# Performance work log

Hardware: AMD Instinct MI355X
Metric: run time of the kernel (lower is better)

Reference implementation:

```python
import jax, jax.numpy as jnp
import numpy as np

NUM_ITEMS = 200000
B = 512
S = 64
D = 64
H = 1
NBLOCKS = 2
EPS = 1e-3  # keras LayerNormalization default epsilon
NEG = -2.0 ** 32 + 1.0  # padding value used by SASRec multihead_attention


def setup_inputs() -> dict:
    key = jax.random.key(0)
    ks = jax.random.split(key, 12)

    def nrm(k, shape, s=0.02):
        return jax.random.normal(k, shape, dtype=jnp.float32) * s

    return {
        "input_ids": jax.random.randint(ks[0], (B, S), 0, NUM_ITEMS + 1),  # id == NUM_ITEMS is padding
        "item_emb": nrm(ks[1], (NUM_ITEMS + 1, D)),
        "pos_emb": nrm(ks[2], (S, D)),
        "ln1_g": jnp.ones((NBLOCKS, D), jnp.float32),
        "ln1_b": jnp.zeros((NBLOCKS, D), jnp.float32),
        "Wq": nrm(ks[3], (NBLOCKS, D, D)),
        "bq": jnp.zeros((NBLOCKS, D), jnp.float32),
        "Wk": nrm(ks[4], (NBLOCKS, D, D)),
        "bk": jnp.zeros((NBLOCKS, D), jnp.float32),
        "Wv": nrm(ks[5], (NBLOCKS, D, D)),
        "bv": jnp.zeros((NBLOCKS, D), jnp.float32),
        "ln2_g": jnp.ones((NBLOCKS, D), jnp.float32),
        "ln2_b": jnp.zeros((NBLOCKS, D), jnp.float32),
        "W1": nrm(ks[6], (NBLOCKS, D, D)),
        "b1": jnp.zeros((NBLOCKS, D), jnp.float32),
        "W2": nrm(ks[7], (NBLOCKS, D, D)),
        "b2": jnp.zeros((NBLOCKS, D), jnp.float32),
        "lnf_g": jnp.ones((D,), jnp.float32),
        "lnf_b": jnp.zeros((D,), jnp.float32),
        "out_item_emb": nrm(ks[8], (NUM_ITEMS, D)),
    }


def _layernorm(x, g, b):
    mu = jnp.mean(x, -1, keepdims=True)
    var = jnp.var(x, -1, keepdims=True)
    return (x - mu) * jax.lax.rsqrt(var + EPS) * g + b


def _mha(queries, keys, Wq, bq, Wk, bk, Wv, bv):
    # SASRec-style multihead attention (inference: dropout disabled).
    # Head split/merge via reshape == tf.split/concat along batch in original.
    Bq, Sq, Dm = queries.shape
    dh = Dm // H

    def split(x):  # [B,S,D] -> [B,H,S,dh]
        return x.reshape(Bq, Sq, H, dh).transpose(0, 2, 1, 3)

    Q = split(queries @ Wq + bq)
    K = split(keys @ Wk + bk)
    V = split(keys @ Wv + bv)
    scores = jnp.einsum('bhqd,bhkd->bhqk', Q, K) / jnp.sqrt(jnp.float32(dh))
    # key masking: padded key positions (all-zero embeddings) get -inf
    key_mask = jnp.sign(jnp.abs(jnp.sum(keys, -1)))  # [B,S]
    scores = jnp.where(key_mask[:, None, None, :] == 0, NEG, scores)
    # causal mask
    causal = jnp.tril(jnp.ones((Sq, Sq), jnp.float32))
    scores = jnp.where(causal[None, None] == 0, NEG, scores)
    attn = jax.nn.softmax(scores, axis=-1)
    # query masking: zero out rows for padded query positions
    query_mask = jnp.sign(jnp.abs(jnp.sum(queries, -1)))  # [B,S]
    attn = attn * query_mask[:, None, :, None]
    out = jnp.einsum('bhqk,bhkd->bhqd', attn, V)
    return out.transpose(0, 2, 1, 3).reshape(Bq, Sq, Dm)


def reference(input_ids, item_emb, pos_emb, ln1_g, ln1_b, Wq, bq, Wk, bk, Wv, bv,
              ln2_g, ln2_b, W1, b1, W2, b2, lnf_g, lnf_b, out_item_emb):
    mask = (input_ids != NUM_ITEMS).astype(jnp.float32)[..., None]  # [B,S,1]
    seq = item_emb[input_ids] + pos_emb[None]                        # [B,S,D]
    seq = seq * mask
    for i in range(NBLOCKS):
        x = _layernorm(seq, ln1_g[i], ln1_b[i])
        q = x
        x = _mha(q, seq, Wq[i], bq[i], Wk[i], bk[i], Wv[i], bv[i])
        x = x + q
        x = _layernorm(x, ln2_g[i], ln2_b[i])
        res = x
        x = jax.nn.relu(x @ W1[i] + b1[i]) @ W2[i] + b2[i]
        x = x + res
        seq = x * mask
    seq_emb = _layernorm(seq, lnf_g, lnf_b)[:, -1, :]  # [B,D]
    # score all items; output activation is linear
    return seq_emb @ out_item_emb.T                    # [B, NUM_ITEMS]
```

## Files before the change

kernel.cpp:

```cpp
#include <hip/hip_runtime.h>
#include <cstddef>


#define NITEMS 200000
#define Bsz 512
#define Ssz 64
#define Dsz 64
#define EPSV 1e-3f
#define NEGV (-4294967295.0f)

typedef __attribute__((ext_vector_type(8))) short short8;
typedef __attribute__((ext_vector_type(4))) float f32x4;
typedef unsigned short ushort_t;
typedef unsigned long long u64_t;

static __device__ __forceinline__ float wsum(float v){
#pragma unroll
  for (int o = 32; o > 0; o >>= 1) v += __shfl_xor(v, o, 64);
  return v;
}
static __device__ __forceinline__ float wmax(float v){
#pragma unroll
  for (int o = 32; o > 0; o >>= 1) v = fmaxf(v, __shfl_xor(v, o, 64));
  return v;
}

static __device__ __forceinline__ ushort_t f2b(float f){
  unsigned u = __float_as_uint(f);
  unsigned r = u + 0x7fffu + ((u >> 16) & 1u);
  return (ushort_t)(r >> 16);
}
static __device__ __forceinline__ float b2f(ushort_t h){
  return __uint_as_float(((unsigned)h) << 16);
}

static __device__ __forceinline__ void a_frag(const float* __restrict__ p,
    short8& h8, short8& l8){
  float4 v0 = *(const float4*)p, v1 = *(const float4*)(p + 4);
  float f[8] = {v0.x,v0.y,v0.z,v0.w,v1.x,v1.y,v1.z,v1.w};
#pragma unroll
  for (int j = 0; j < 8; ++j){
    ushort_t hh = f2b(f[j]);
    h8[j] = (short)hh;
    l8[j] = (short)f2b(f[j] - b2f(hh));
  }
}

__global__ __launch_bounds__(512) void k_packw(const float* __restrict__ Wq,
    const float* __restrict__ Wk, const float* __restrict__ Wv,
    const float* __restrict__ W1, const float* __restrict__ W2,
    short8* __restrict__ Wp){
  const int m = blockIdx.x;
  const int l = m / 5, which = m % 5;
  const float* Ws[5] = {Wq, Wk, Wv, W1, W2};
  const float* Wg = Ws[which] + l * 4096;
  const int t = threadIdx.x;
  const int lane = t & 63, s = t >> 6;
  const int li = lane & 15, g = lane >> 4;
  const int cb = s >> 1, kc = s & 1;
  short8 h, lo;
#pragma unroll
  for (int j = 0; j < 8; ++j){
    float f = Wg[(kc*32 + g*8 + j)*64 + cb*16 + li];
    ushort_t hh = f2b(f);
    h[j] = (short)hh;
    lo[j] = (short)f2b(f - b2f(hh));
  }
  Wp[(m*16 + s)*64 + lane] = h;
  Wp[(m*16 + 8 + s)*64 + lane] = lo;
}

static __device__ __forceinline__ void mmW2p(const short8 ah[2], const short8 al[2],
    const short8* __restrict__ Wp, int m, int cbh, int lane, f32x4 acc[2]){
#pragma unroll
  for (int nt = 0; nt < 2; ++nt){
    acc[nt] = (f32x4)(0.f);
#pragma unroll
    for (int kc = 0; kc < 2; ++kc){
      int s = (cbh*2 + nt)*2 + kc;
      short8 bh = Wp[(m*16 + s)*64 + lane];
      short8 bl = Wp[(m*16 + 8 + s)*64 + lane];
      acc[nt] = __builtin_amdgcn_mfma_f32_16x16x32_bf16(ah[kc], bh, acc[nt], 0, 0, 0);
      acc[nt] = __builtin_amdgcn_mfma_f32_16x16x32_bf16(ah[kc], bl, acc[nt], 0, 0, 0);
      acc[nt] = __builtin_amdgcn_mfma_f32_16x16x32_bf16(al[kc], bh, acc[nt], 0, 0, 0);
    }
  }
}

static __device__ __forceinline__ void mmB2(const short8 ah[2], const short8 al[2],
    const float (*__restrict__ B)[68], int cbh, int li, int g, f32x4 acc[2]){
#pragma unroll
  for (int nt = 0; nt < 2; ++nt){
    acc[nt] = (f32x4)(0.f);
#pragma unroll
    for (int kc = 0; kc < 2; ++kc){
      short8 bh, bl;
      a_frag(&B[cbh*32 + nt*16 + li][kc*32 + g*8], bh, bl);
      acc[nt] = __builtin_amdgcn_mfma_f32_16x16x32_bf16(ah[kc], bh, acc[nt], 0, 0, 0);
      acc[nt] = __builtin_amdgcn_mfma_f32_16x16x32_bf16(ah[kc], bl, acc[nt], 0, 0, 0);
      acc[nt] = __builtin_amdgcn_mfma_f32_16x16x32_bf16(al[kc], bh, acc[nt], 0, 0, 0);
    }
  }
}

__global__ __launch_bounds__(512, 4) void k_layers(const int* __restrict__ ids,
    const float* __restrict__ item_emb, const float* __restrict__ pos_emb,
    const float* __restrict__ ln1g, const float* __restrict__ ln1b,
    const short8* __restrict__ Wp,
    const float* __restrict__ bq, const float* __restrict__ bk,
    const float* __restrict__ bv,
    const float* __restrict__ ln2g, const float* __restrict__ ln2b,
    const float* __restrict__ b1, const float* __restrict__ b2,
    const float* __restrict__ lnfg, const float* __restrict__ lnfb,
    ushort_t* __restrict__ Eh, ushort_t* __restrict__ El){
  __shared__ float B0[64][68];
  __shared__ float B1[64][68];
  __shared__ float B2[64][68];
  __shared__ float B3[64][68];

  const int t = threadIdx.x;
  const int lane = t & 63, wid = t >> 6;
  const int li = lane & 15, g = lane >> 4;
  const int qb = wid & 3, cbh = wid >> 2;
  const int b = blockIdx.x;

#pragma unroll
  for (int it = 0; it < 2; ++it){
    int e4 = t + 512 * it;
    int r = e4 >> 4, c4 = e4 & 15, c = c4 * 4;
    int id = ids[b * Ssz + r];
    float4 v = make_float4(0.f, 0.f, 0.f, 0.f);
    if (id != NITEMS){
      float4 a = ((const float4*)(item_emb + (size_t)id * 64))[c4];
      float4 p = ((const float4*)(pos_emb + r * 64))[c4];
      v = make_float4(a.x + p.x, a.y + p.y, a.z + p.z, a.w + p.w);
    }
    *(float4*)&B0[r][c] = v;
  }
  const int myid = ids[b * Ssz + lane];
  const u64_t mvec = __ballot(myid != NITEMS);

  for (int l = 0; l < 2; ++l){
    const int mb = l * 5;
    __syncthreads();

    for (int r = wid; r < 64; r += 8){
      float x = B0[r][lane];
      float mu = wsum(x) * (1.f / 64.f);
      float dv = x - mu;
      float var = wsum(dv * dv) * (1.f / 64.f);
      B1[r][lane] = dv * (1.f / sqrtf(var + EPSV)) * ln1g[l*64 + lane] + ln1b[l*64 + lane];
    }
    __syncthreads();

    short8 a0h[2], a0l[2], a1h[2], a1l[2];
#pragma unroll
    for (int kc = 0; kc < 2; ++kc){
      a_frag(&B0[qb*16 + li][kc*32 + g*8], a0h[kc], a0l[kc]);
      a_frag(&B1[qb*16 + li][kc*32 + g*8], a1h[kc], a1l[kc]);
    }
    { f32x4 acc[2]; mmW2p(a1h, a1l, Wp, mb + 0, cbh, lane, acc);
#pragma unroll
      for (int nt = 0; nt < 2; ++nt){
        int col = cbh*32 + nt*16 + li; float bb = bq[l*64 + col];
#pragma unroll
        for (int r4 = 0; r4 < 4; ++r4) B2[qb*16 + g*4 + r4][col] = acc[nt][r4] + bb;
      }
    }
    { f32x4 acc[2]; mmW2p(a0h, a0l, Wp, mb + 1, cbh, lane, acc);
#pragma unroll
      for (int nt = 0; nt < 2; ++nt){
        int col = cbh*32 + nt*16 + li; float bb = bk[l*64 + col];
#pragma unroll
        for (int r4 = 0; r4 < 4; ++r4) B3[qb*16 + g*4 + r4][col] = acc[nt][r4] + bb;
      }
    }
    __syncthreads();

    { f32x4 acc[2]; mmW2p(a0h, a0l, Wp, mb + 2, cbh, lane, acc);
#pragma unroll
      for (int nt = 0; nt < 2; ++nt){
        int col = cbh*32 + nt*16 + li; float bb = bv[l*64 + col];
#pragma unroll
        for (int r4 = 0; r4 < 4; ++r4) B0[col][qb*16 + g*4 + r4] = acc[nt][r4] + bb;
      }
    }
    short8 qh[2], ql[2];
#pragma unroll
    for (int kc = 0; kc < 2; ++kc)
      a_frag(&B2[qb*16 + li][kc*32 + g*8], qh[kc], ql[kc]);
    __syncthreads();

    { f32x4 acc[2]; mmB2(qh, ql, B3, cbh, li, g, acc);
#pragma unroll
      for (int nt = 0; nt < 2; ++nt){
        int col = cbh*32 + nt*16 + li;
#pragma unroll
        for (int r4 = 0; r4 < 4; ++r4) B2[qb*16 + g*4 + r4][col] = acc[nt][r4];
      }
    }
    __syncthreads();

    for (int r = wid; r < 64; r += 8){
      float raw = B2[r][lane];
      bool valid = (lane <= r) && ((mvec >> lane) & 1);
      float sc = valid ? raw * 0.125f : NEGV;
      float m = wmax(sc);
      float e = __expf(sc - m);
      float ssumv = wsum(e);
      float qm = ((mvec >> r) & 1) ? 1.f : 0.f;
      B2[r][lane] = (e / ssumv) * qm;
    }
    __syncthreads();

    { short8 pfh[2], pfl[2];
#pragma unroll
      for (int kc = 0; kc < 2; ++kc)
        a_frag(&B2[qb*16 + li][kc*32 + g*8], pfh[kc], pfl[kc]);
      f32x4 acc[2]; mmB2(pfh, pfl, B0, cbh, li, g, acc);
#pragma unroll
      for (int nt = 0; nt < 2; ++nt){
        int col = cbh*32 + nt*16 + li;
#pragma unroll
        for (int r4 = 0; r4 < 4; ++r4){
          int row = qb*16 + g*4 + r4;
          B3[row][col] = acc[nt][r4] + B1[row][col];
        }
      }
    }
    __syncthreads();

    for (int r = wid; r < 64; r += 8){
      float x = B3[r][lane];
      float mu = wsum(x) * (1.f / 64.f);
      float dv = x - mu;
      float var = wsum(dv * dv) * (1.f / 64.f);
      B1[r][lane] = dv * (1.f / sqrtf(var + EPSV)) * ln2g[l*64 + lane] + ln2b[l*64 + lane];
    }
    __syncthreads();

    { short8 rh[2], rl[2];
#pragma unroll
      for (int kc = 0; kc < 2; ++kc)
        a_frag(&B1[qb*16 + li][kc*32 + g*8], rh[kc], rl[kc]);
      f32x4 acc[2]; mmW2p(rh, rl, Wp, mb + 3, cbh, lane, acc);
#pragma unroll
      for (int nt = 0; nt < 2; ++nt){
        int col = cbh*32 + nt*16 + li; float bb = b1[l*64 + col];
#pragma unroll
        for (int r4 = 0; r4 < 4; ++r4)
          B2[qb*16 + g*4 + r4][col] = fmaxf(acc[nt][r4] + bb, 0.f);
      }
    }
    __syncthreads();

    { short8 hh[2], hl[2];
#pragma unroll
      for (int kc = 0; kc < 2; ++kc)
        a_frag(&B2[qb*16 + li][kc*32 + g*8], hh[kc], hl[kc]);
      f32x4 acc[2]; mmW2p(hh, hl, Wp, mb + 4, cbh, lane, acc);
#pragma unroll
      for (int nt = 0; nt < 2; ++nt){
        int col = cbh*32 + nt*16 + li; float bb = b2[l*64 + col];
#pragma unroll
        for (int r4 = 0; r4 < 4; ++r4){
          int row = qb*16 + g*4 + r4;
          float m = ((mvec >> row) & 1) ? 1.f : 0.f;
          B0[row][col] = (acc[nt][r4] + bb + B1[row][col]) * m;
        }
      }
    }
  }

  __syncthreads();
  if (wid == 0){
    float x = B0[63][lane];
    float mu = wsum(x) * (1.f / 64.f);
    float dv = x - mu;
    float var = wsum(dv * dv) * (1.f / 64.f);
    float o = dv * (1.f / sqrtf(var + EPSV)) * lnfg[lane] + lnfb[lane];
    ushort_t h = f2b(o);
    Eh[b * 64 + lane] = h;
    El[b * 64 + lane] = f2b(o - b2f(h));
  }
}

#define LOADA(DH, DL, c) { int er = (c)*64 + w*16 + li;                 \
  DH[0] = *(const short8*)&Eh[er*64 + g*8];                             \
  DH[1] = *(const short8*)&Eh[er*64 + 32 + g*8];                        \
  DL[0] = *(const short8*)&El[er*64 + g*8];                             \
  DL[1] = *(const short8*)&El[er*64 + 32 + g*8]; }

#define CHUNK(c, CAh, CAl, NAh, NAl, PF) {                              \
  if (PF) LOADA(NAh, NAl, (c)+1);                                       \
  f32x4 acc[8];                                                         \
  _Pragma("unroll") for (int nt = 0; nt < 8; ++nt) acc[nt] = (f32x4)(0.f); \
  _Pragma("unroll") for (int kc = 0; kc < 2; ++kc){                     \
    _Pragma("unroll") for (int nt = 0; nt < 8; ++nt){                   \
      short8 bh = TB[nt*2 + kc][lane];                                  \
      short8 bl = TB[16 + nt*2 + kc][lane];                             \
      acc[nt] = __builtin_amdgcn_mfma_f32_16x16x32_bf16(CAh[kc], bh, acc[nt], 0, 0, 0); \
      acc[nt] = __builtin_amdgcn_mfma_f32_16x16x32_bf16(CAh[kc], bl, acc[nt], 0, 0, 0); \
      acc[nt] = __builtin_amdgcn_mfma_f32_16x16x32_bf16(CAl[kc], bh, acc[nt], 0, 0, 0); \
    }}                                                                  \
  _Pragma("unroll") for (int nt = 0; nt < 8; ++nt)                      \
    _Pragma("unroll") for (int r = 0; r < 4; ++r)                       \
      TT[w][g*4 + r][nt*16 + li] = acc[nt][r];                          \
  asm volatile("s_waitcnt lgkmcnt(0)" ::: "memory");                    \
  __builtin_amdgcn_sched_barrier(0);                                    \
  _Pragma("unroll") for (int k = 0; k < 4; ++k){                        \
    int rr = 4*k + g;                                                   \
    size_t rb = (size_t)((c)*64 + w*16 + rr) * NITEMS;                  \
    _Pragma("unroll") for (int h2 = 0; h2 < 2; ++h2){                   \
      int cidx = (h2*16 + li) * 4;                                      \
      int col = i0 + cidx;                                              \
      if (col < NITEMS){                                                \
        f32x4 v = *(const f32x4*)&TT[w][rr][cidx];                      \
        __builtin_nontemporal_store(v, (f32x4*)&out[rb + col]);         \
      }                                                                 \
    }}                                                                  \
  __builtin_amdgcn_sched_barrier(0); }

__global__ __launch_bounds__(256) void k_score(
    const ushort_t* __restrict__ Eh, const ushort_t* __restrict__ El,
    const float* __restrict__ T, float* __restrict__ out){
  __shared__ short8 TB[32][64];
  __shared__ float TT[4][16][132];
  const int t = threadIdx.x, lane = t & 63, w = t >> 6;
  const int li = lane & 15, g = lane >> 4;
  const int i0 = blockIdx.x * 128;

#pragma unroll
  for (int i = 0; i < 8; ++i){
    int e4 = t + 256 * i;
    int r = e4 >> 4, c4 = e4 & 15;
    int gi = i0 + r;
    float4 v = make_float4(0.f, 0.f, 0.f, 0.f);
    if (gi < NITEMS) v = ((const float4*)(T + (size_t)gi * 64))[c4];
    int nt = r >> 4, li2 = r & 15;
    int kc = c4 >> 3, g2 = (c4 >> 1) & 3, j0 = (c4 & 1) * 4;
    float f[4] = {v.x, v.y, v.z, v.w};
    u64_t ph = 0, pl = 0;
#pragma unroll
    for (int j = 0; j < 4; ++j){
      ushort_t hh = f2b(f[j]);
      ushort_t ll = f2b(f[j] - b2f(hh));
      ph |= (u64_t)hh << (16*j);
      pl |= (u64_t)ll << (16*j);
    }
    *(u64_t*)((ushort_t*)&TB[nt*2 + kc][g2*16 + li2] + j0) = ph;
    *(u64_t*)((ushort_t*)&TB[16 + nt*2 + kc][g2*16 + li2] + j0) = pl;
  }
  __syncthreads();

  short8 Ah0[2], Al0[2], Ah1[2], Al1[2];
  LOADA(Ah0, Al0, 0);
  CHUNK(0, Ah0, Al0, Ah1, Al1, 1)
  CHUNK(1, Ah1, Al1, Ah0, Al0, 1)
  CHUNK(2, Ah0, Al0, Ah1, Al1, 1)
  CHUNK(3, Ah1, Al1, Ah0, Al0, 1)
  CHUNK(4, Ah0, Al0, Ah1, Al1, 1)
  CHUNK(5, Ah1, Al1, Ah0, Al0, 1)
  CHUNK(6, Ah0, Al0, Ah1, Al1, 1)
  CHUNK(7, Ah1, Al1, Ah0, Al0, 0)
}

extern "C" void kernel_launch(void* const* d_in, const int* in_sizes, int n_in,
                              void* d_out, int out_size, void* d_ws, size_t ws_size,
                              hipStream_t stream){
  const int*   ids      = (const int*)  d_in[0];
  const float* item_emb = (const float*)d_in[1];
  const float* pos_emb  = (const float*)d_in[2];
  const float* ln1g     = (const float*)d_in[3];
  const float* ln1b     = (const float*)d_in[4];
  const float* Wq       = (const float*)d_in[5];
  const float* bq       = (const float*)d_in[6];
  const float* Wk       = (const float*)d_in[7];
  const float* bk       = (const float*)d_in[8];
  const float* Wv       = (const float*)d_in[9];
  const float* bv       = (const float*)d_in[10];
  const float* ln2g     = (const float*)d_in[11];
  const float* ln2b     = (const float*)d_in[12];
  const float* W1       = (const float*)d_in[13];
  const float* b1       = (const float*)d_in[14];
  const float* W2       = (const float*)d_in[15];
  const float* b2       = (const float*)d_in[16];
  const float* lnfg     = (const float*)d_in[17];
  const float* lnfb     = (const float*)d_in[18];
  const float* items    = (const float*)d_in[19];
  float* out = (float*)d_out;

  ushort_t* Ehp = (ushort_t*)d_ws;
  ushort_t* Elp = Ehp + 512 * 64;
  short8*   Wp  = (short8*)((char*)d_ws + (256u << 10));

  k_packw<<<10, 512, 0, stream>>>(Wq, Wk, Wv, W1, W2, Wp);
  k_layers<<<Bsz, 512, 0, stream>>>(ids, item_emb, pos_emb,
      ln1g, ln1b, Wp, bq, bk, bv,
      ln2g, ln2b, b1, b2, lnfg, lnfb, Ehp, Elp);
  k_score<<<1563, 256, 0, stream>>>(Ehp, Elp, items, out);
}
```

Before: 155.8 us.

## Compute only the last query row in the final transformer block

The second block now computes K and V for all 64 positions with MFMA, but handles the query path, attention, LayerNorm, FFN and final LayerNorm only for the last position, since only that row feeds the scoring. That row runs in a single wavefront using shuffle-based fp32 matvecs read directly from the unpacked weights. This removes most of the second block's query, FFN and norm work per sequence, at the cost of a serial single-wave tail with 64-step shuffle loops.

New measurement: 176.7 us. 13.5% more time.

```diff
diff --git a/kernel.cpp b/kernel.cpp
--- a/kernel.cpp
+++ b/kernel.cpp
@@ -107,6 +107,8 @@
     const float* __restrict__ item_emb, const float* __restrict__ pos_emb,
     const float* __restrict__ ln1g, const float* __restrict__ ln1b,
     const short8* __restrict__ Wp,
+    const float* __restrict__ Wqf, const float* __restrict__ W1f,
+    const float* __restrict__ W2f,
     const float* __restrict__ bq, const float* __restrict__ bk,
     const float* __restrict__ bv,
     const float* __restrict__ ln2g, const float* __restrict__ ln2b,
@@ -140,8 +142,8 @@
   const int myid = ids[b * Ssz + lane];
   const u64_t mvec = __ballot(myid != NITEMS);
 
-  for (int l = 0; l < 2; ++l){
-    const int mb = l * 5;
+  {
+    const int l = 0, mb = 0;
     __syncthreads();
 
     for (int r = wid; r < 64; r += 8){
@@ -273,15 +275,84 @@
   }
 
   __syncthreads();
+
+  {
+    short8 s0h[2], s0l[2];
+#pragma unroll
+    for (int kc = 0; kc < 2; ++kc)
+      a_frag(&B0[qb*16 + li][kc*32 + g*8], s0h[kc], s0l[kc]);
+    { f32x4 acc[2]; mmW2p(s0h, s0l, Wp, 5 + 1, cbh, lane, acc);
+#pragma unroll
+      for (int nt = 0; nt < 2; ++nt){
+        int col = cbh*32 + nt*16 + li; float bb = bk[64 + col];
+#pragma unroll
+        for (int r4 = 0; r4 < 4; ++r4) B3[col][qb*16 + g*4 + r4] = acc[nt][r4] + bb;
+      }
+    }
+    { f32x4 acc[2]; mmW2p(s0h, s0l, Wp, 5 + 2, cbh, lane, acc);
+#pragma unroll
+      for (int nt = 0; nt < 2; ++nt){
+        int col = cbh*32 + nt*16 + li; float bb = bv[64 + col];
+#pragma unroll
+        for (int r4 = 0; r4 < 4; ++r4) B2[qb*16 + g*4 + r4][col] = acc[nt][r4] + bb;
+      }
+    }
+  }
+  __syncthreads();
+
   if (wid == 0){
     float x = B0[63][lane];
     float mu = wsum(x) * (1.f / 64.f);
     float dv = x - mu;
     float var = wsum(dv * dv) * (1.f / 64.f);
-    float o = dv * (1.f / sqrtf(var + EPSV)) * lnfg[lane] + lnfb[lane];
-    ushort_t h = f2b(o);
-    Eh[b * 64 + lane] = h;
-    El[b * 64 + lane] = f2b(o - b2f(h));
+    float xq = dv * (1.f / sqrtf(var + EPSV)) * ln1g[64 + lane] + ln1b[64 + lane];
+
+    float q = bq[64 + lane];
+#pragma unroll
+    for (int k = 0; k < 64; ++k)
+      q = fmaf(__shfl(xq, k), Wqf[4096 + k*64 + lane], q);
+
+    float raw = 0.f;
+#pragma unroll
+    for (int k = 0; k < 64; ++k)
+      raw = fmaf(__shfl(q, k), B3[k][lane], raw);
+    bool kvalid = (mvec >> lane) & 1;
+    float sc = kvalid ? raw * 0.125f : NEGV;
+    float m = wmax(sc);
+    float e = __expf(sc - m);
+    float ssumv = wsum(e);
+    float qm = (mvec >> 63) ? 1.f : 0.f;
+    float p = (e / ssumv) * qm;
+
+    float o = 0.f;
+#pragma unroll
+    for (int j = 0; j < 64; ++j)
+      o = fmaf(__shfl(p, j), B2[j][lane], o);
+    float x2 = o + xq;
+
+    float mu2 = wsum(x2) * (1.f / 64.f);
+    float dv2 = x2 - mu2;
+    float var2 = wsum(dv2 * dv2) * (1.f / 64.f);
+    float res = dv2 * (1.f / sqrtf(var2 + EPSV)) * ln2g[64 + lane] + ln2b[64 + lane];
+
+    float h = b1[64 + lane];
+#pragma unroll
+    for (int k = 0; k < 64; ++k)
+      h = fmaf(__shfl(res, k), W1f[4096 + k*64 + lane], h);
+    h = fmaxf(h, 0.f);
+    float o2 = b2[64 + lane];
+#pragma unroll
+    for (int k = 0; k < 64; ++k)
+      o2 = fmaf(__shfl(h, k), W2f[4096 + k*64 + lane], o2);
+    o2 = (o2 + res) * qm;
+
+    float mu3 = wsum(o2) * (1.f / 64.f);
+    float dv3 = o2 - mu3;
+    float var3 = wsum(dv3 * dv3) * (1.f / 64.f);
+    float ef = dv3 * (1.f / sqrtf(var3 + EPSV)) * lnfg[lane] + lnfb[lane];
+    ushort_t hh = f2b(ef);
+    Eh[b * 64 + lane] = hh;
+    El[b * 64 + lane] = f2b(ef - b2f(hh));
   }
 }
 
@@ -396,7 +467,7 @@
 
   k_packw<<<10, 512, 0, stream>>>(Wq, Wk, Wv, W1, W2, Wp);
   k_layers<<<Bsz, 512, 0, stream>>>(ids, item_emb, pos_emb,
-      ln1g, ln1b, Wp, bq, bk, bv,
+      ln1g, ln1b, Wp, Wq, W1, W2, bq, bk, bv,
       ln2g, ln2b, b1, b2, lnfg, lnfb, Ehp, Elp);
   k_score<<<1563, 256, 0, stream>>>(Ehp, Elp, items, out);
 }
```

## Process two sequences per block, each wave owning all output columns

Applied to the files above, without the earlier changes.

The layers kernel now handles two batch sequences per 512-thread block instead of one. Four waves serve each sequence, and each wave computes all 64 output columns for its 16-row strip instead of half of them. LDS buffers double to hold both sequences, the grid halves to 256 blocks, and launch bounds drop to 2 blocks per CU. The aim is to raise per-wave MFMA work and A-fragment reuse while reducing block count and redundant A-fragment loads. In exchange the larger LDS footprint and lower occupancy may reduce latency hiding.

New measurement: 174.5 us. 12.0% more time.

```diff
diff --git a/kernel.cpp b/kernel.cpp
--- a/kernel.cpp
+++ b/kernel.cpp
@@ -70,14 +70,14 @@
   Wp[(m*16 + 8 + s)*64 + lane] = lo;
 }
 
-static __device__ __forceinline__ void mmW2p(const short8 ah[2], const short8 al[2],
-    const short8* __restrict__ Wp, int m, int cbh, int lane, f32x4 acc[2]){
-#pragma unroll
-  for (int nt = 0; nt < 2; ++nt){
+static __device__ __forceinline__ void mmW4p(const short8 ah[2], const short8 al[2],
+    const short8* __restrict__ Wp, int m, int lane, f32x4 acc[4]){
+#pragma unroll
+  for (int nt = 0; nt < 4; ++nt){
     acc[nt] = (f32x4)(0.f);
 #pragma unroll
     for (int kc = 0; kc < 2; ++kc){
-      int s = (cbh*2 + nt)*2 + kc;
+      int s = nt*2 + kc;
       short8 bh = Wp[(m*16 + s)*64 + lane];
       short8 bl = Wp[(m*16 + 8 + s)*64 + lane];
       acc[nt] = __builtin_amdgcn_mfma_f32_16x16x32_bf16(ah[kc], bh, acc[nt], 0, 0, 0);
@@ -87,15 +87,15 @@
   }
 }
 
-static __device__ __forceinline__ void mmB2(const short8 ah[2], const short8 al[2],
-    const float (*__restrict__ B)[68], int cbh, int li, int g, f32x4 acc[2]){
-#pragma unroll
-  for (int nt = 0; nt < 2; ++nt){
+static __device__ __forceinline__ void mmB4(const short8 ah[2], const short8 al[2],
+    const float (*__restrict__ B)[68], int li, int g, f32x4 acc[4]){
+#pragma unroll
+  for (int nt = 0; nt < 4; ++nt){
     acc[nt] = (f32x4)(0.f);
 #pragma unroll
     for (int kc = 0; kc < 2; ++kc){
       short8 bh, bl;
-      a_frag(&B[cbh*32 + nt*16 + li][kc*32 + g*8], bh, bl);
+      a_frag(&B[nt*16 + li][kc*32 + g*8], bh, bl);
       acc[nt] = __builtin_amdgcn_mfma_f32_16x16x32_bf16(ah[kc], bh, acc[nt], 0, 0, 0);
       acc[nt] = __builtin_amdgcn_mfma_f32_16x16x32_bf16(ah[kc], bl, acc[nt], 0, 0, 0);
       acc[nt] = __builtin_amdgcn_mfma_f32_16x16x32_bf16(al[kc], bh, acc[nt], 0, 0, 0);
@@ -103,7 +103,7 @@
   }
 }
 
-__global__ __launch_bounds__(512, 4) void k_layers(const int* __restrict__ ids,
+__global__ __launch_bounds__(512, 2) void k_layers(const int* __restrict__ ids,
     const float* __restrict__ item_emb, const float* __restrict__ pos_emb,
     const float* __restrict__ ln1g, const float* __restrict__ ln1b,
     const short8* __restrict__ Wp,
@@ -113,143 +113,143 @@
     const float* __restrict__ b1, const float* __restrict__ b2,
     const float* __restrict__ lnfg, const float* __restrict__ lnfb,
     ushort_t* __restrict__ Eh, ushort_t* __restrict__ El){
-  __shared__ float B0[64][68];
-  __shared__ float B1[64][68];
-  __shared__ float B2[64][68];
-  __shared__ float B3[64][68];
+  __shared__ float B0[2][64][68];
+  __shared__ float B1[2][64][68];
+  __shared__ float B2[2][64][68];
+  __shared__ float B3[2][64][68];
 
   const int t = threadIdx.x;
   const int lane = t & 63, wid = t >> 6;
   const int li = lane & 15, g = lane >> 4;
-  const int qb = wid & 3, cbh = wid >> 2;
+  const int sq = wid >> 2, qb = wid & 3;
   const int b = blockIdx.x;
 
 #pragma unroll
-  for (int it = 0; it < 2; ++it){
+  for (int it = 0; it < 4; ++it){
     int e4 = t + 512 * it;
-    int r = e4 >> 4, c4 = e4 & 15, c = c4 * 4;
-    int id = ids[b * Ssz + r];
+    int s2 = e4 >> 10, r = (e4 >> 4) & 63, c4 = e4 & 15, c = c4 * 4;
+    int id = ids[(b*2 + s2) * Ssz + r];
     float4 v = make_float4(0.f, 0.f, 0.f, 0.f);
     if (id != NITEMS){
       float4 a = ((const float4*)(item_emb + (size_t)id * 64))[c4];
       float4 p = ((const float4*)(pos_emb + r * 64))[c4];
       v = make_float4(a.x + p.x, a.y + p.y, a.z + p.z, a.w + p.w);
     }
-    *(float4*)&B0[r][c] = v;
-  }
-  const int myid = ids[b * Ssz + lane];
+    *(float4*)&B0[s2][r][c] = v;
+  }
+  const int myid = ids[(b*2 + sq) * Ssz + lane];
   const u64_t mvec = __ballot(myid != NITEMS);
 
   for (int l = 0; l < 2; ++l){
     const int mb = l * 5;
     __syncthreads();
 
-    for (int r = wid; r < 64; r += 8){
-      float x = B0[r][lane];
+    for (int r = qb; r < 64; r += 4){
+      float x = B0[sq][r][lane];
       float mu = wsum(x) * (1.f / 64.f);
       float dv = x - mu;
       float var = wsum(dv * dv) * (1.f / 64.f);
-      B1[r][lane] = dv * (1.f / sqrtf(var + EPSV)) * ln1g[l*64 + lane] + ln1b[l*64 + lane];
+      B1[sq][r][lane] = dv * (1.f / sqrtf(var + EPSV)) * ln1g[l*64 + lane] + ln1b[l*64 + lane];
     }
     __syncthreads();
 
     short8 a0h[2], a0l[2], a1h[2], a1l[2];
 #pragma unroll
     for (int kc = 0; kc < 2; ++kc){
-      a_frag(&B0[qb*16 + li][kc*32 + g*8], a0h[kc], a0l[kc]);
-      a_frag(&B1[qb*16 + li][kc*32 + g*8], a1h[kc], a1l[kc]);
-    }
-    { f32x4 acc[2]; mmW2p(a1h, a1l, Wp, mb + 0, cbh, lane, acc);
-#pragma unroll
-      for (int nt = 0; nt < 2; ++nt){
-        int col = cbh*32 + nt*16 + li; float bb = bq[l*64 + col];
-#pragma unroll
-        for (int r4 = 0; r4 < 4; ++r4) B2[qb*16 + g*4 + r4][col] = acc[nt][r4] + bb;
-      }
-    }
-    { f32x4 acc[2]; mmW2p(a0h, a0l, Wp, mb + 1, cbh, lane, acc);
-#pragma unroll
-      for (int nt = 0; nt < 2; ++nt){
-        int col = cbh*32 + nt*16 + li; float bb = bk[l*64 + col];
-#pragma unroll
-        for (int r4 = 0; r4 < 4; ++r4) B3[qb*16 + g*4 + r4][col] = acc[nt][r4] + bb;
-      }
-    }
-    __syncthreads();
-
-    { f32x4 acc[2]; mmW2p(a0h, a0l, Wp, mb + 2, cbh, lane, acc);
-#pragma unroll
-      for (int nt = 0; nt < 2; ++nt){
-        int col = cbh*32 + nt*16 + li; float bb = bv[l*64 + col];
-#pragma unroll
-        for (int r4 = 0; r4 < 4; ++r4) B0[col][qb*16 + g*4 + r4] = acc[nt][r4] + bb;
+      a_frag(&B0[sq][qb*16 + li][kc*32 + g*8], a0h[kc], a0l[kc]);
+      a_frag(&B1[sq][qb*16 + li][kc*32 + g*8], a1h[kc], a1l[kc]);
+    }
+    { f32x4 acc[4]; mmW4p(a1h, a1l, Wp, mb + 0, lane, acc);
+#pragma unroll
+      for (int nt = 0; nt < 4; ++nt){
+        int col = nt*16 + li; float bb = bq[l*64 + col];
+#pragma unroll
+        for (int r4 = 0; r4 < 4; ++r4) B2[sq][qb*16 + g*4 + r4][col] = acc[nt][r4] + bb;
+      }
+    }
+    { f32x4 acc[4]; mmW4p(a0h, a0l, Wp, mb + 1, lane, acc);
+#pragma unroll
+      for (int nt = 0; nt < 4; ++nt){
+        int col = nt*16 + li; float bb = bk[l*64 + col];
+#pragma unroll
+        for (int r4 = 0; r4 < 4; ++r4) B3[sq][qb*16 + g*4 + r4][col] = acc[nt][r4] + bb;
+      }
+    }
+    __syncthreads();
+
+    { f32x4 acc[4]; mmW4p(a0h, a0l, Wp, mb + 2, lane, acc);
+#pragma unroll
+      for (int nt = 0; nt < 4; ++nt){
+        int col = nt*16 + li; float bb = bv[l*64 + col];
+#pragma unroll
+        for (int r4 = 0; r4 < 4; ++r4) B0[sq][col][qb*16 + g*4 + r4] = acc[nt][r4] + bb;
       }
     }
     short8 qh[2], ql[2];
 #pragma unroll
     for (int kc = 0; kc < 2; ++kc)
-      a_frag(&B2[qb*16 + li][kc*32 + g*8], qh[kc], ql[kc]);
-    __syncthreads();
-
-    { f32x4 acc[2]; mmB2(qh, ql, B3, cbh, li, g, acc);
-#pragma unroll
-      for (int nt = 0; nt < 2; ++nt){
-        int col = cbh*32 + nt*16 + li;
-#pragma unroll
-        for (int r4 = 0; r4 < 4; ++r4) B2[qb*16 + g*4 + r4][col] = acc[nt][r4];
-      }
-    }
-    __syncthreads();
-
-    for (int r = wid; r < 64; r += 8){
-      float raw = B2[r][lane];
+      a_frag(&B2[sq][qb*16 + li][kc*32 + g*8], qh[kc], ql[kc]);
+    __syncthreads();
+
+    { f32x4 acc[4]; mmB4(qh, ql, B3[sq], li, g, acc);
+#pragma unroll
+      for (int nt = 0; nt < 4; ++nt){
+        int col = nt*16 + li;
+#pragma unroll
+        for (int r4 = 0; r4 < 4; ++r4) B2[sq][qb*16 + g*4 + r4][col] = acc[nt][r4];
+      }
+    }
+    __syncthreads();
+
+    for (int r = qb; r < 64; r += 4){
+      float raw = B2[sq][r][lane];
       bool valid = (lane <= r) && ((mvec >> lane) & 1);
       float sc = valid ? raw * 0.125f : NEGV;
       float m = wmax(sc);
       float e = __expf(sc - m);
       float ssumv = wsum(e);
       float qm = ((mvec >> r) & 1) ? 1.f : 0.f;
-      B2[r][lane] = (e / ssumv) * qm;
+      B2[sq][r][lane] = (e / ssumv) * qm;
     }
     __syncthreads();
 
     { short8 pfh[2], pfl[2];
 #pragma unroll
       for (int kc = 0; kc < 2; ++kc)
-        a_frag(&B2[qb*16 + li][kc*32 + g*8], pfh[kc], pfl[kc]);
-      f32x4 acc[2]; mmB2(pfh, pfl, B0, cbh, li, g, acc);
-#pragma unroll
-      for (int nt = 0; nt < 2; ++nt){
-        int col = cbh*32 + nt*16 + li;
+        a_frag(&B2[sq][qb*16 + li][kc*32 + g*8], pfh[kc], pfl[kc]);
+      f32x4 acc[4]; mmB4(pfh, pfl, B0[sq], li, g, acc);
+#pragma unroll
+      for (int nt = 0; nt < 4; ++nt){
+        int col = nt*16 + li;
 #pragma unroll
         for (int r4 = 0; r4 < 4; ++r4){
           int row = qb*16 + g*4 + r4;
-          B3[row][col] = acc[nt][r4] + B1[row][col];
+          B3[sq][row][col] = acc[nt][r4] + B1[sq][row][col];
         }
       }
     }
     __syncthreads();
 
-    for (int r = wid; r < 64; r += 8){
-      float x = B3[r][lane];
+    for (int r = qb; r < 64; r += 4){
+      float x = B3[sq][r][lane];
       float mu = wsum(x) * (1.f / 64.f);
       float dv = x - mu;
       float var = wsum(dv * dv) * (1.f / 64.f);
-      B1[r][lane] = dv * (1.f / sqrtf(var + EPSV)) * ln2g[l*64 + lane] + ln2b[l*64 + lane];
+      B1[sq][r][lane] = dv * (1.f / sqrtf(var + EPSV)) * ln2g[l*64 + lane] + ln2b[l*64 + lane];
     }
     __syncthreads();
 
     { short8 rh[2], rl[2];
 #pragma unroll
       for (int kc = 0; kc < 2; ++kc)
-        a_frag(&B1[qb*16 + li][kc*32 + g*8], rh[kc], rl[kc]);
-      f32x4 acc[2]; mmW2p(rh, rl, Wp, mb + 3, cbh, lane, acc);
-#pragma unroll
-      for (int nt = 0; nt < 2; ++nt){
-        int col = cbh*32 + nt*16 + li; float bb = b1[l*64 + col];
+        a_frag(&B1[sq][qb*16 + li][kc*32 + g*8], rh[kc], rl[kc]);
+      f32x4 acc[4]; mmW4p(rh, rl, Wp, mb + 3, lane, acc);
+#pragma unroll
+      for (int nt = 0; nt < 4; ++nt){
+        int col = nt*16 + li; float bb = b1[l*64 + col];
 #pragma unroll
         for (int r4 = 0; r4 < 4; ++r4)
-          B2[qb*16 + g*4 + r4][col] = fmaxf(acc[nt][r4] + bb, 0.f);
+          B2[sq][qb*16 + g*4 + r4][col] = fmaxf(acc[nt][r4] + bb, 0.f);
       }
     }
     __syncthreads();
@@ -257,31 +257,31 @@
     { short8 hh[2], hl[2];
 #pragma unroll
       for (int kc = 0; kc < 2; ++kc)
-        a_frag(&B2[qb*16 + li][kc*32 + g*8], hh[kc], hl[kc]);
-      f32x4 acc[2]; mmW2p(hh, hl, Wp, mb + 4, cbh, lane, acc);
-#pragma unroll
-      for (int nt = 0; nt < 2; ++nt){
-        int col = cbh*32 + nt*16 + li; float bb = b2[l*64 + col];
+        a_frag(&B2[sq][qb*16 + li][kc*32 + g*8], hh[kc], hl[kc]);
+      f32x4 acc[4]; mmW4p(hh, hl, Wp, mb + 4, lane, acc);
+#pragma unroll
+      for (int nt = 0; nt < 4; ++nt){
+        int col = nt*16 + li; float bb = b2[l*64 + col];
 #pragma unroll
         for (int r4 = 0; r4 < 4; ++r4){
           int row = qb*16 + g*4 + r4;
           float m = ((mvec >> row) & 1) ? 1.f : 0.f;
-          B0[row][col] = (acc[nt][r4] + bb + B1[row][col]) * m;
+          B0[sq][row][col] = (acc[nt][r4] + bb + B1[sq][row][col]) * m;
         }
       }
     }
   }
 
   __syncthreads();
-  if (wid == 0){
-    float x = B0[63][lane];
+  if (qb == 0){
+    float x = B0[sq][63][lane];
     float mu = wsum(x) * (1.f / 64.f);
     float dv = x - mu;
     float var = wsum(dv * dv) * (1.f / 64.f);
     float o = dv * (1.f / sqrtf(var + EPSV)) * lnfg[lane] + lnfb[lane];
     ushort_t h = f2b(o);
-    Eh[b * 64 + lane] = h;
-    El[b * 64 + lane] = f2b(o - b2f(h));
+    Eh[(b*2 + sq) * 64 + lane] = h;
+    El[(b*2 + sq) * 64 + lane] = f2b(o - b2f(h));
   }
 }
 
@@ -395,7 +395,7 @@
   short8*   Wp  = (short8*)((char*)d_ws + (256u << 10));
 
   k_packw<<<10, 512, 0, stream>>>(Wq, Wk, Wv, W1, W2, Wp);
-  k_layers<<<Bsz, 512, 0, stream>>>(ids, item_emb, pos_emb,
+  k_layers<<<256, 512, 0, stream>>>(ids, item_emb, pos_emb,
       ln1g, ln1b, Wp, bq, bk, bv,
       ln2g, ln2b, b1, b2, lnfg, lnfb, Ehp, Elp);
   k_score<<<1563, 256, 0, stream>>>(Ehp, Elp, items, out);
```
